# Optimization experiments

Hardware: AMD Instinct MI355X
Metric: run time of the kernel (lower is better)

## Reference

```python
import jax, jax.numpy as jnp
import numpy as np

N_NODES = 20000
N_EDGES = 320000
NUM_FEAT = 14
DIM = 256


def setup_inputs() -> dict:
    key = jax.random.key(0)
    ks = jax.random.split(key, 12)
    x = jax.random.normal(ks[0], (N_NODES, NUM_FEAT), dtype=jnp.float32)
    edge_index = jax.random.randint(ks[1], (2, N_EDGES), 0, N_NODES, dtype=jnp.int64)
    edge_weight = jax.random.uniform(ks[2], (N_EDGES,), dtype=jnp.float32)

    def lin_w(k, fan_in, fan_out):
        b = 1.0 / np.sqrt(fan_in)
        return jax.random.uniform(k, (fan_in, fan_out), jnp.float32, -b, b)

    params = {
        'W1_rel': lin_w(ks[3], NUM_FEAT, DIM), 'b1_rel': jnp.zeros((DIM,), jnp.float32),
        'W1_root': lin_w(ks[4], NUM_FEAT, DIM),
        'W2_rel': lin_w(ks[5], DIM, DIM), 'b2_rel': jnp.zeros((DIM,), jnp.float32),
        'W2_root': lin_w(ks[6], DIM, DIM),
        'W3_rel': lin_w(ks[7], DIM, DIM), 'b3_rel': jnp.zeros((DIM,), jnp.float32),
        'W3_root': lin_w(ks[8], DIM, DIM),
        'W_lin': lin_w(ks[9], 3 * DIM, DIM), 'b_lin': jnp.zeros((DIM,), jnp.float32),
    }
    return {'x': x, 'edge_index': edge_index, 'edge_weight': edge_weight, **params}


def _graph_conv(x, src, dst, ew, W_rel, b_rel, W_root, n_nodes):
    # message: x_j * w_ij ; aggr='mean' over incoming edges (count, not weight sum)
    msg = x[src] * ew[:, None]                               # [E, F]
    agg = jax.ops.segment_sum(msg, dst, num_segments=n_nodes)  # [N, F]
    cnt = jax.ops.segment_sum(jnp.ones_like(ew), dst, num_segments=n_nodes)
    mean = agg / jnp.maximum(cnt, 1.0)[:, None]
    return mean @ W_rel + b_rel + x @ W_root


def reference(x, edge_index, edge_weight,
              W1_rel, b1_rel, W1_root,
              W2_rel, b2_rel, W2_root,
              W3_rel, b3_rel, W3_root,
              W_lin, b_lin):
    src, dst = edge_index[0], edge_index[1]
    n = x.shape[0]
    # eval mode: dropout is identity
    x1 = jax.nn.relu(_graph_conv(x, src, dst, edge_weight, W1_rel, b1_rel, W1_root, n))
    x2 = jax.nn.relu(_graph_conv(x1, src, dst, edge_weight, W2_rel, b2_rel, W2_root, n))
    x3 = jax.nn.relu(_graph_conv(x2, src, dst, edge_weight, W3_rel, b3_rel, W3_root, n))
    xc = jnp.concatenate([x1, x2, x3], axis=-1)              # [N, 3*DIM]
    return xc @ W_lin + b_lin
```

## Files before the change

kernel.cpp:

```cpp
#include <hip/hip_runtime.h>

#define N_NODES 20000
#define N_EDGES 320000
#define NFEAT 14
#define DIM 256

typedef short bf16x8 __attribute__((ext_vector_type(8)));
typedef float f32x4 __attribute__((ext_vector_type(4)));

__device__ __forceinline__ float b2f(unsigned short u) {
    union { unsigned int u; float f; } v; v.u = ((unsigned int)u) << 16; return v.f;
}
__device__ __forceinline__ unsigned short f2b(float f) {
    union { float f; unsigned int u; } v; v.f = f;
    unsigned int r = v.u + 0x7fffu + ((v.u >> 16) & 1u);
    return (unsigned short)(r >> 16);
}


__global__ __launch_bounds__(256) void k_degree(const int* __restrict__ ei, int* __restrict__ cnt) {
    int e = blockIdx.x * 256 + threadIdx.x;
    if (e < N_EDGES) atomicAdd(&cnt[ei[N_EDGES + e]], 1);
}

__global__ __launch_bounds__(256) void k_alloc(const int* __restrict__ cnt,
                                               int* __restrict__ total,
                                               int* __restrict__ row_ptr,
                                               int* __restrict__ cursor) {
    int i = blockIdx.x * 256 + threadIdx.x;
    int lane = threadIdx.x & 63;
    int deg = (i < N_NODES) ? cnt[i] : 0;
    int s = deg;
    for (int o = 1; o < 64; o <<= 1) { int t = __shfl_up(s, o); if (lane >= o) s += t; }
    int wsum = __shfl(s, 63);
    int base = 0;
    if (lane == 63) base = atomicAdd(total, wsum);
    base = __shfl(base, 63);
    int excl = base + s - deg;
    if (i < N_NODES) { row_ptr[i] = excl; cursor[i] = excl; }
}

__global__ __launch_bounds__(256) void k_fill(const int* __restrict__ ei, const float* __restrict__ ew,
                                              int* __restrict__ cursor,
                                              int* __restrict__ csr_src, float* __restrict__ csr_w) {
    int e = blockIdx.x * 256 + threadIdx.x;
    if (e < N_EDGES) {
        int d = ei[N_EDGES + e];
        int p = atomicAdd(&cursor[d], 1);
        csr_src[p] = ei[e];
        csr_w[p] = ew[e];
    }
}


__global__ __launch_bounds__(256) void k_wstage(
    const float* __restrict__ W2r, const float* __restrict__ W2o,
    const float* __restrict__ W3r, const float* __restrict__ W3o,
    const float* __restrict__ Wl, unsigned short* __restrict__ out) {
    __shared__ unsigned short tb[256][33];
    int part = blockIdx.x >> 3, s = blockIdx.x & 7;
    int tid = threadIdx.x;
    const float* W; int koff = 0;
    switch (part) {
        case 0: W = W2r; break;
        case 1: W = W2o; break;
        case 2: W = W3r; break;
        case 3: W = W3o; break;
        default: W = Wl; koff = (part - 4) * 256; break;
    }
#pragma unroll 4
    for (int j = 0; j < 32; ++j) {
        tb[tid][j] = f2b(W[(size_t)(koff + s * 32 + j) * 256 + tid]);
    }
    __syncthreads();
    unsigned short* dst = out + (size_t)part * 65536 + (size_t)s * 8192;
#pragma unroll 4
    for (int i = 0; i < 32; ++i) {
        int flat = i * 256 + tid;
        dst[flat] = tb[flat >> 5][flat & 31];
    }
}


__global__ __launch_bounds__(256) void k_agg14(
    const float* __restrict__ x, const int* __restrict__ row_ptr, const int* __restrict__ cnt,
    const int* __restrict__ csr_src, const float* __restrict__ csr_w,
    float* __restrict__ agg) {
    int t = blockIdx.x * 256 + threadIdx.x;
    int node = t >> 4, k = t & 15;
    int start = row_ptr[node], deg = cnt[node], end = start + deg;
    bool kv = (k < NFEAT);
    float acc = 0.f;
    for (int e0 = start; e0 < end; e0 += 4) {
        int rem = end - e0;
        int s0 = csr_src[e0];                    float w0 = csr_w[e0];
        int s1 = (rem > 1) ? csr_src[e0 + 1] : s0; float w1 = (rem > 1) ? csr_w[e0 + 1] : 0.f;
        int s2 = (rem > 2) ? csr_src[e0 + 2] : s0; float w2 = (rem > 2) ? csr_w[e0 + 2] : 0.f;
        int s3 = (rem > 3) ? csr_src[e0 + 3] : s0; float w3 = (rem > 3) ? csr_w[e0 + 3] : 0.f;
        if (kv) {
            float x0 = x[(size_t)s0 * NFEAT + k];
            float x1 = x[(size_t)s1 * NFEAT + k];
            float x2 = x[(size_t)s2 * NFEAT + k];
            float x3 = x[(size_t)s3 * NFEAT + k];
            acc += x0 * w0 + x1 * w1 + x2 * w2 + x3 * w3;
        }
    }
    agg[(size_t)node * 16 + k] = kv ? acc / fmaxf((float)deg, 1.f) : 0.f;
}


__global__ __launch_bounds__(256) void k_l1dense(
    const float* __restrict__ x, const float* __restrict__ agg,
    const float* __restrict__ Wrel, const float* __restrict__ brel,
    const float* __restrict__ Wroot, unsigned short* __restrict__ x1b) {
    __shared__ float sWrel[NFEAT][DIM];
    __shared__ float sWroot[NFEAT][DIM];
    __shared__ float sb[DIM];
    int tid = threadIdx.x;
    for (int i = tid; i < NFEAT * DIM; i += 256) {
        (&sWrel[0][0])[i] = Wrel[i];
        (&sWroot[0][0])[i] = Wroot[i];
    }
    if (tid < DIM) sb[tid] = brel[tid];
    __syncthreads();

    int wv = tid >> 6, lane = tid & 63;
    for (int n8 = 0; n8 < 8; ++n8) {
        int node = blockIdx.x * 32 + n8 * 4 + wv;
        float av[NFEAT], xr[NFEAT];
        const float4* ag4 = (const float4*)(agg + (size_t)node * 16);
        float4 a0 = ag4[0], a1 = ag4[1], a2 = ag4[2], a3 = ag4[3];
        av[0]=a0.x; av[1]=a0.y; av[2]=a0.z; av[3]=a0.w;
        av[4]=a1.x; av[5]=a1.y; av[6]=a1.z; av[7]=a1.w;
        av[8]=a2.x; av[9]=a2.y; av[10]=a2.z; av[11]=a2.w;
        av[12]=a3.x; av[13]=a3.y;
        const float2* xr2 = (const float2*)(x + (size_t)node * NFEAT);
#pragma unroll
        for (int k2 = 0; k2 < 7; ++k2) { float2 v = xr2[k2]; xr[2*k2] = v.x; xr[2*k2+1] = v.y; }

#pragma unroll
        for (int j = 0; j < 4; ++j) {
            int d = lane + 64 * j;
            float o = sb[d];
#pragma unroll
            for (int k2 = 0; k2 < NFEAT; ++k2)
                o += av[k2] * sWrel[k2][d] + xr[k2] * sWroot[k2][d];
            x1b[(size_t)node * DIM + d] = f2b(fmaxf(o, 0.f));
        }
    }
}


__global__ __launch_bounds__(256) void k_spmm_mean(
    const unsigned short* __restrict__ xin, const int* __restrict__ row_ptr,
    const int* __restrict__ cnt, const int* __restrict__ csr_src,
    const float* __restrict__ csr_w, unsigned short* __restrict__ meanb) {
    int wv = threadIdx.x >> 6, lane = threadIdx.x & 63;
    int node = blockIdx.x * 4 + wv;
    int start = row_ptr[node], deg = cnt[node], end = start + deg;
    float a0 = 0.f, a1 = 0.f, a2 = 0.f, a3 = 0.f;
    for (int e0 = start; e0 < end; e0 += 4) {
        int rem = end - e0;
        int s0 = csr_src[e0];                    float w0 = csr_w[e0];
        int s1 = (rem > 1) ? csr_src[e0 + 1] : s0; float w1 = (rem > 1) ? csr_w[e0 + 1] : 0.f;
        int s2 = (rem > 2) ? csr_src[e0 + 2] : s0; float w2 = (rem > 2) ? csr_w[e0 + 2] : 0.f;
        int s3 = (rem > 3) ? csr_src[e0 + 3] : s0; float w3 = (rem > 3) ? csr_w[e0 + 3] : 0.f;
        ushort4 v0 = *(const ushort4*)(xin + (size_t)s0 * DIM + lane * 4);
        ushort4 v1 = *(const ushort4*)(xin + (size_t)s1 * DIM + lane * 4);
        ushort4 v2 = *(const ushort4*)(xin + (size_t)s2 * DIM + lane * 4);
        ushort4 v3 = *(const ushort4*)(xin + (size_t)s3 * DIM + lane * 4);
        a0 += b2f(v0.x) * w0 + b2f(v1.x) * w1 + b2f(v2.x) * w2 + b2f(v3.x) * w3;
        a1 += b2f(v0.y) * w0 + b2f(v1.y) * w1 + b2f(v2.y) * w2 + b2f(v3.y) * w3;
        a2 += b2f(v0.z) * w0 + b2f(v1.z) * w1 + b2f(v2.z) * w2 + b2f(v3.z) * w3;
        a3 += b2f(v0.w) * w0 + b2f(v1.w) * w1 + b2f(v2.w) * w2 + b2f(v3.w) * w3;
    }
    float inv = 1.f / fmaxf((float)deg, 1.f);
    ushort4 o;
    o.x = f2b(a0 * inv); o.y = f2b(a1 * inv); o.z = f2b(a2 * inv); o.w = f2b(a3 * inv);
    *(ushort4*)(meanb + (size_t)node * DIM + lane * 4) = o;
}


__global__ __launch_bounds__(256) void k_gemm_mfma(
    const unsigned short* __restrict__ A0, const unsigned short* __restrict__ A1,
    const unsigned short* __restrict__ A2,
    const unsigned short* __restrict__ B0, const unsigned short* __restrict__ B1,
    const unsigned short* __restrict__ B2,
    int nparts, const float* __restrict__ bias,
    unsigned short* __restrict__ outb, float* __restrict__ outf, int do_relu) {
    __shared__ __align__(16) unsigned short Bs[256][40];
    int t = threadIdx.x;
    int l = t & 63, wv = t >> 6;
    int rowPanel = wv >> 1, colPanel = wv & 1;
    int row0 = blockIdx.x * 32;
    int lr = l & 15, kg = l >> 4;
    int row_a = row0 + rowPanel * 16 + lr;

    f32x4 acc[8];
#pragma unroll
    for (int i = 0; i < 8; i++) acc[i] = (f32x4){0.f, 0.f, 0.f, 0.f};

    for (int p = 0; p < nparts; ++p) {
        const unsigned short* A = (p == 0) ? A0 : (p == 1) ? A1 : A2;
        const unsigned short* B = (p == 0) ? B0 : (p == 1) ? B1 : B2;
        for (int s = 0; s < 8; ++s) {
            const int4* src = (const int4*)(B + (size_t)s * 8192 + (size_t)t * 32);
            int4 v0 = src[0], v1 = src[1], v2 = src[2], v3 = src[3];
            *(int4*)&Bs[t][0]  = v0;
            *(int4*)&Bs[t][8]  = v1;
            *(int4*)&Bs[t][16] = v2;
            *(int4*)&Bs[t][24] = v3;
            __syncthreads();
            bf16x8 a = *(const bf16x8*)(A + (size_t)row_a * DIM + s * 32 + kg * 8);
#pragma unroll
            for (int ct = 0; ct < 8; ++ct) {
                int col = colPanel * 128 + ct * 16 + lr;
                bf16x8 b = *(const bf16x8*)&Bs[col][kg * 8];
                acc[ct] = __builtin_amdgcn_mfma_f32_16x16x32_bf16(a, b, acc[ct], 0, 0, 0);
            }
            __syncthreads();
        }
    }

#pragma unroll
    for (int ct = 0; ct < 8; ++ct) {
        int col = colPanel * 128 + ct * 16 + lr;
        float bv = bias[col];
#pragma unroll
        for (int r = 0; r < 4; ++r) {
            int row = row0 + rowPanel * 16 + kg * 4 + r;
            float v = acc[ct][r] + bv;
            if (do_relu) v = fmaxf(v, 0.f);
            if (outb) outb[(size_t)row * DIM + col] = f2b(v);
            else      outf[(size_t)row * DIM + col] = v;
        }
    }
}


extern "C" void kernel_launch(void* const* d_in, const int* in_sizes, int n_in,
                              void* d_out, int out_size, void* d_ws, size_t ws_size,
                              hipStream_t stream) {
    (void)in_sizes; (void)n_in; (void)out_size; (void)ws_size;
    const float* x       = (const float*)d_in[0];
    const int*   ei      = (const int*)d_in[1];
    const float* ew      = (const float*)d_in[2];
    const float* W1_rel  = (const float*)d_in[3];
    const float* b1      = (const float*)d_in[4];
    const float* W1_root = (const float*)d_in[5];
    const float* W2_rel  = (const float*)d_in[6];
    const float* b2      = (const float*)d_in[7];
    const float* W2_root = (const float*)d_in[8];
    const float* W3_rel  = (const float*)d_in[9];
    const float* b3      = (const float*)d_in[10];
    const float* W3_root = (const float*)d_in[11];
    const float* W_lin   = (const float*)d_in[12];
    const float* b_lin   = (const float*)d_in[13];
    float* out = (float*)d_out;

    char* ws = (char*)d_ws;
    size_t off = 0;
    auto alloc = [&](size_t bytes) -> void* {
        off = (off + 255) & ~(size_t)255;
        void* p = ws + off;
        off += bytes;
        return p;
    };
    int*   cnt     = (int*)alloc((size_t)(N_NODES + 1) * 4);
    int*   row_ptr = (int*)alloc((size_t)N_NODES * 4);
    int*   cursor  = (int*)alloc((size_t)N_NODES * 4);
    int*   csr_src = (int*)alloc((size_t)N_EDGES * 4);
    float* csr_w   = (float*)alloc((size_t)N_EDGES * 4);
    float* agg     = (float*)alloc((size_t)N_NODES * 16 * 4);
    unsigned short* wst   = (unsigned short*)alloc((size_t)7 * 65536 * 2);
    unsigned short* meanb = (unsigned short*)alloc((size_t)N_NODES * DIM * 2);
    unsigned short* x1b   = (unsigned short*)alloc((size_t)N_NODES * DIM * 2);
    unsigned short* x2b   = (unsigned short*)alloc((size_t)N_NODES * DIM * 2);
    unsigned short* x3b   = (unsigned short*)alloc((size_t)N_NODES * DIM * 2);
    int* total = cnt + N_NODES;

    hipMemsetAsync(cnt, 0, (size_t)(N_NODES + 1) * 4, stream);

    int eblocks = (N_EDGES + 255) / 256;
    k_degree<<<eblocks, 256, 0, stream>>>(ei, cnt);
    k_alloc<<<(N_NODES + 255) / 256, 256, 0, stream>>>(cnt, total, row_ptr, cursor);
    k_fill<<<eblocks, 256, 0, stream>>>(ei, ew, cursor, csr_src, csr_w);

    k_wstage<<<56, 256, 0, stream>>>(W2_rel, W2_root, W3_rel, W3_root, W_lin, wst);

    k_agg14<<<N_NODES * 16 / 256, 256, 0, stream>>>(x, row_ptr, cnt, csr_src, csr_w, agg);
    k_l1dense<<<N_NODES / 32, 256, 0, stream>>>(x, agg, W1_rel, b1, W1_root, x1b);

    const int ggrid = N_NODES / 32;

    k_spmm_mean<<<N_NODES / 4, 256, 0, stream>>>(x1b, row_ptr, cnt, csr_src, csr_w, meanb);
    k_gemm_mfma<<<ggrid, 256, 0, stream>>>(meanb, x1b, nullptr,
                                           wst, wst + 65536, nullptr,
                                           2, b2, x2b, nullptr, 1);

    k_spmm_mean<<<N_NODES / 4, 256, 0, stream>>>(x2b, row_ptr, cnt, csr_src, csr_w, meanb);
    k_gemm_mfma<<<ggrid, 256, 0, stream>>>(meanb, x2b, nullptr,
                                           wst + 2 * 65536, wst + 3 * 65536, nullptr,
                                           2, b3, x3b, nullptr, 1);

    k_gemm_mfma<<<ggrid, 256, 0, stream>>>(x1b, x2b, x3b,
                                           wst + 4 * 65536, wst + 5 * 65536, wst + 6 * 65536,
                                           3, b_lin, nullptr, out, 0);
}
```

Baseline: 287.8 us.

## Fuse neighbor mean aggregation into the layer GEMM via shared memory

Merges the sparse mean aggregation and the dense MFMA GEMM of layers 2 and 3 into one kernel. Each block aggregates its 32 nodes into an LDS tile, with half-wavefronts loading 16-byte chunks, then multiplies that tile by the weights, so the bf16 mean buffer is never written to or read back from global memory. This removes two launches and the intermediate traffic. In exchange the gather now runs with far fewer blocks (625 instead of 5000) and is load-imbalanced across the 32 nodes of a block, which may reduce latency hiding on the irregular gather.

```diff
diff --git a/kernel.cpp b/kernel.cpp
--- a/kernel.cpp
+++ b/kernel.cpp
@@ -6,6 +6,7 @@
 #define DIM 256
 
 typedef short bf16x8 __attribute__((ext_vector_type(8)));
+typedef unsigned short u16x8 __attribute__((ext_vector_type(8)));
 typedef float f32x4 __attribute__((ext_vector_type(4)));
 
 __device__ __forceinline__ float b2f(unsigned short u) {
@@ -151,33 +152,90 @@
 }
 
 
-__global__ __launch_bounds__(256) void k_spmm_mean(
-    const unsigned short* __restrict__ xin, const int* __restrict__ row_ptr,
+__global__ __launch_bounds__(256) void k_layer_fused(
+    const unsigned short* __restrict__ xprev, const int* __restrict__ row_ptr,
     const int* __restrict__ cnt, const int* __restrict__ csr_src,
-    const float* __restrict__ csr_w, unsigned short* __restrict__ meanb) {
-    int wv = threadIdx.x >> 6, lane = threadIdx.x & 63;
-    int node = blockIdx.x * 4 + wv;
-    int start = row_ptr[node], deg = cnt[node], end = start + deg;
-    float a0 = 0.f, a1 = 0.f, a2 = 0.f, a3 = 0.f;
-    for (int e0 = start; e0 < end; e0 += 4) {
-        int rem = end - e0;
-        int s0 = csr_src[e0];                    float w0 = csr_w[e0];
-        int s1 = (rem > 1) ? csr_src[e0 + 1] : s0; float w1 = (rem > 1) ? csr_w[e0 + 1] : 0.f;
-        int s2 = (rem > 2) ? csr_src[e0 + 2] : s0; float w2 = (rem > 2) ? csr_w[e0 + 2] : 0.f;
-        int s3 = (rem > 3) ? csr_src[e0 + 3] : s0; float w3 = (rem > 3) ? csr_w[e0 + 3] : 0.f;
-        ushort4 v0 = *(const ushort4*)(xin + (size_t)s0 * DIM + lane * 4);
-        ushort4 v1 = *(const ushort4*)(xin + (size_t)s1 * DIM + lane * 4);
-        ushort4 v2 = *(const ushort4*)(xin + (size_t)s2 * DIM + lane * 4);
-        ushort4 v3 = *(const ushort4*)(xin + (size_t)s3 * DIM + lane * 4);
-        a0 += b2f(v0.x) * w0 + b2f(v1.x) * w1 + b2f(v2.x) * w2 + b2f(v3.x) * w3;
-        a1 += b2f(v0.y) * w0 + b2f(v1.y) * w1 + b2f(v2.y) * w2 + b2f(v3.y) * w3;
-        a2 += b2f(v0.z) * w0 + b2f(v1.z) * w1 + b2f(v2.z) * w2 + b2f(v3.z) * w3;
-        a3 += b2f(v0.w) * w0 + b2f(v1.w) * w1 + b2f(v2.w) * w2 + b2f(v3.w) * w3;
-    }
-    float inv = 1.f / fmaxf((float)deg, 1.f);
-    ushort4 o;
-    o.x = f2b(a0 * inv); o.y = f2b(a1 * inv); o.z = f2b(a2 * inv); o.w = f2b(a3 * inv);
-    *(ushort4*)(meanb + (size_t)node * DIM + lane * 4) = o;
+    const float* __restrict__ csr_w,
+    const unsigned short* __restrict__ Brel, const unsigned short* __restrict__ Broot,
+    const float* __restrict__ bias, unsigned short* __restrict__ outb) {
+    __shared__ __align__(16) unsigned short As[32][264];
+    __shared__ __align__(16) unsigned short Bs[256][40];
+    int t = threadIdx.x;
+    int l = t & 63, wv = t >> 6;
+    int node0 = blockIdx.x * 32;
+
+    {
+        int half = l >> 5;
+        int c8 = l & 31;
+        for (int p = 0; p < 4; ++p) {
+            int local = wv * 8 + p * 2 + half;
+            int node = node0 + local;
+            int start = row_ptr[node], deg = cnt[node], end = start + deg;
+            float acc[8] = {0.f,0.f,0.f,0.f,0.f,0.f,0.f,0.f};
+            for (int e0 = start; e0 < end; e0 += 4) {
+                int rem = end - e0;
+                int s0 = csr_src[e0];                    float w0 = csr_w[e0];
+                int s1 = (rem > 1) ? csr_src[e0 + 1] : s0; float w1 = (rem > 1) ? csr_w[e0 + 1] : 0.f;
+                int s2 = (rem > 2) ? csr_src[e0 + 2] : s0; float w2 = (rem > 2) ? csr_w[e0 + 2] : 0.f;
+                int s3 = (rem > 3) ? csr_src[e0 + 3] : s0; float w3 = (rem > 3) ? csr_w[e0 + 3] : 0.f;
+                u16x8 v0 = *(const u16x8*)(xprev + (size_t)s0 * DIM + c8 * 8);
+                u16x8 v1 = *(const u16x8*)(xprev + (size_t)s1 * DIM + c8 * 8);
+                u16x8 v2 = *(const u16x8*)(xprev + (size_t)s2 * DIM + c8 * 8);
+                u16x8 v3 = *(const u16x8*)(xprev + (size_t)s3 * DIM + c8 * 8);
+#pragma unroll
+                for (int i = 0; i < 8; ++i)
+                    acc[i] += b2f(v0[i]) * w0 + b2f(v1[i]) * w1 + b2f(v2[i]) * w2 + b2f(v3[i]) * w3;
+            }
+            float inv = 1.f / fmaxf((float)deg, 1.f);
+            u16x8 r;
+#pragma unroll
+            for (int i = 0; i < 8; ++i) r[i] = f2b(acc[i] * inv);
+            *(u16x8*)&As[local][c8 * 8] = r;
+        }
+    }
+
+    int rowPanel = wv >> 1, colPanel = wv & 1;
+    int lr = l & 15, kg = l >> 4;
+    int row_l = rowPanel * 16 + lr;
+
+    f32x4 acc[8];
+#pragma unroll
+    for (int i = 0; i < 8; i++) acc[i] = (f32x4){0.f, 0.f, 0.f, 0.f};
+
+    for (int p = 0; p < 2; ++p) {
+        const unsigned short* B = (p == 0) ? Brel : Broot;
+        for (int s = 0; s < 8; ++s) {
+            const int4* src = (const int4*)(B + (size_t)s * 8192 + (size_t)t * 32);
+            int4 v0 = src[0], v1 = src[1], v2 = src[2], v3 = src[3];
+            *(int4*)&Bs[t][0]  = v0;
+            *(int4*)&Bs[t][8]  = v1;
+            *(int4*)&Bs[t][16] = v2;
+            *(int4*)&Bs[t][24] = v3;
+            __syncthreads();
+            bf16x8 a;
+            if (p == 0) a = *(const bf16x8*)&As[row_l][s * 32 + kg * 8];
+            else        a = *(const bf16x8*)(xprev + (size_t)(node0 + row_l) * DIM + s * 32 + kg * 8);
+#pragma unroll
+            for (int ct = 0; ct < 8; ++ct) {
+                int col = colPanel * 128 + ct * 16 + lr;
+                bf16x8 b = *(const bf16x8*)&Bs[col][kg * 8];
+                acc[ct] = __builtin_amdgcn_mfma_f32_16x16x32_bf16(a, b, acc[ct], 0, 0, 0);
+            }
+            __syncthreads();
+        }
+    }
+
+#pragma unroll
+    for (int ct = 0; ct < 8; ++ct) {
+        int col = colPanel * 128 + ct * 16 + lr;
+        float bv = bias[col];
+#pragma unroll
+        for (int r = 0; r < 4; ++r) {
+            int row = node0 + rowPanel * 16 + kg * 4 + r;
+            float v = fmaxf(acc[ct][r] + bv, 0.f);
+            outb[(size_t)row * DIM + col] = f2b(v);
+        }
+    }
 }
 
 
@@ -186,8 +244,7 @@
     const unsigned short* __restrict__ A2,
     const unsigned short* __restrict__ B0, const unsigned short* __restrict__ B1,
     const unsigned short* __restrict__ B2,
-    int nparts, const float* __restrict__ bias,
-    unsigned short* __restrict__ outb, float* __restrict__ outf, int do_relu) {
+    const float* __restrict__ bias, float* __restrict__ outf) {
     __shared__ __align__(16) unsigned short Bs[256][40];
     int t = threadIdx.x;
     int l = t & 63, wv = t >> 6;
@@ -200,7 +257,7 @@
 #pragma unroll
     for (int i = 0; i < 8; i++) acc[i] = (f32x4){0.f, 0.f, 0.f, 0.f};
 
-    for (int p = 0; p < nparts; ++p) {
+    for (int p = 0; p < 3; ++p) {
         const unsigned short* A = (p == 0) ? A0 : (p == 1) ? A1 : A2;
         const unsigned short* B = (p == 0) ? B0 : (p == 1) ? B1 : B2;
         for (int s = 0; s < 8; ++s) {
@@ -229,10 +286,7 @@
 #pragma unroll
         for (int r = 0; r < 4; ++r) {
             int row = row0 + rowPanel * 16 + kg * 4 + r;
-            float v = acc[ct][r] + bv;
-            if (do_relu) v = fmaxf(v, 0.f);
-            if (outb) outb[(size_t)row * DIM + col] = f2b(v);
-            else      outf[(size_t)row * DIM + col] = v;
+            outf[(size_t)row * DIM + col] = acc[ct][r] + bv;
         }
     }
 }
@@ -272,11 +326,10 @@
     int*   csr_src = (int*)alloc((size_t)N_EDGES * 4);
     float* csr_w   = (float*)alloc((size_t)N_EDGES * 4);
     float* agg     = (float*)alloc((size_t)N_NODES * 16 * 4);
-    unsigned short* wst   = (unsigned short*)alloc((size_t)7 * 65536 * 2);
-    unsigned short* meanb = (unsigned short*)alloc((size_t)N_NODES * DIM * 2);
-    unsigned short* x1b   = (unsigned short*)alloc((size_t)N_NODES * DIM * 2);
-    unsigned short* x2b   = (unsigned short*)alloc((size_t)N_NODES * DIM * 2);
-    unsigned short* x3b   = (unsigned short*)alloc((size_t)N_NODES * DIM * 2);
+    unsigned short* wst = (unsigned short*)alloc((size_t)7 * 65536 * 2);
+    unsigned short* x1b = (unsigned short*)alloc((size_t)N_NODES * DIM * 2);
+    unsigned short* x2b = (unsigned short*)alloc((size_t)N_NODES * DIM * 2);
+    unsigned short* x3b = (unsigned short*)alloc((size_t)N_NODES * DIM * 2);
     int* total = cnt + N_NODES;
 
     hipMemsetAsync(cnt, 0, (size_t)(N_NODES + 1) * 4, stream);
@@ -293,17 +346,12 @@
 
     const int ggrid = N_NODES / 32;
 
-    k_spmm_mean<<<N_NODES / 4, 256, 0, stream>>>(x1b, row_ptr, cnt, csr_src, csr_w, meanb);
-    k_gemm_mfma<<<ggrid, 256, 0, stream>>>(meanb, x1b, nullptr,
-                                           wst, wst + 65536, nullptr,
-                                           2, b2, x2b, nullptr, 1);
-
-    k_spmm_mean<<<N_NODES / 4, 256, 0, stream>>>(x2b, row_ptr, cnt, csr_src, csr_w, meanb);
-    k_gemm_mfma<<<ggrid, 256, 0, stream>>>(meanb, x2b, nullptr,
-                                           wst + 2 * 65536, wst + 3 * 65536, nullptr,
-                                           2, b3, x3b, nullptr, 1);
+    k_layer_fused<<<ggrid, 256, 0, stream>>>(x1b, row_ptr, cnt, csr_src, csr_w,
+                                             wst, wst + 65536, b2, x2b);
+    k_layer_fused<<<ggrid, 256, 0, stream>>>(x2b, row_ptr, cnt, csr_src, csr_w,
+                                             wst + 2 * 65536, wst + 3 * 65536, b3, x3b);
 
     k_gemm_mfma<<<ggrid, 256, 0, stream>>>(x1b, x2b, x3b,
                                            wst + 4 * 65536, wst + 5 * 65536, wst + 6 * 65536,
-                                           3, b_lin, nullptr, out, 0);
-}
+                                           b_lin, out);
+}
```

Measured after the change: 291.7 us. About the same (+1.4%).
